# Kernel tuning notes

Measured on AMD Instinct MI355X. Metric: run time of the kernel, lower is better.

## Reference

```python
import jax, jax.numpy as jnp
import numpy as np

N_NODES = 100000
N_EDGES = 1600000
N_GRAPHS = 256
F_IN = 128
HID = 128


def gcn_conv(x, W, b, src, dst, n_nodes):
    """PyG GCNConv: h = D^{-1/2}(A+I)D^{-1/2} (x @ W) + b, self-loops added."""
    h = x @ W  # [N, H]
    ones = jnp.ones((src.shape[0],), dtype=x.dtype)
    deg = jax.ops.segment_sum(ones, dst, num_segments=n_nodes) + 1.0  # +1 self-loop
    dinv = jax.lax.rsqrt(deg)  # deg >= 1 always
    norm = dinv[src] * dinv[dst]  # [E]
    msgs = h[src] * norm[:, None]  # gather + scale, [E, H]
    agg = jax.ops.segment_sum(msgs, dst, num_segments=n_nodes)  # scatter-add
    agg = agg + h * (dinv * dinv)[:, None]  # self-loop contribution
    return agg + b


def setup_inputs() -> dict:
    key = jax.random.key(0)
    ks = jax.random.split(key, 8)
    x = jax.random.normal(ks[0], (N_NODES, F_IN), dtype=jnp.float32)
    edge_index = jax.random.randint(ks[1], (2, N_EDGES), 0, N_NODES, dtype=jnp.int64)
    batch = jnp.sort(jax.random.randint(ks[2], (N_NODES,), 0, N_GRAPHS, dtype=jnp.int64))
    s1 = 1.0 / np.sqrt(F_IN)
    s2 = 1.0 / np.sqrt(HID)
    w1 = jax.random.normal(ks[3], (F_IN, HID), dtype=jnp.float32) * s1
    b1 = jnp.zeros((HID,), dtype=jnp.float32)
    w2 = jax.random.normal(ks[4], (HID, HID), dtype=jnp.float32) * s2
    b2 = jnp.zeros((HID,), dtype=jnp.float32)
    w_out = jax.random.normal(ks[5], (HID, 1), dtype=jnp.float32) * s2
    b_out = jnp.zeros((1,), dtype=jnp.float32)
    return {"x": x, "edge_index": edge_index, "batch": batch,
            "w1": w1, "b1": b1, "w2": w2, "b2": b2,
            "w_out": w_out, "b_out": b_out}


def reference(x, edge_index, batch, w1, b1, w2, b2, w_out, b_out):
    src, dst = edge_index[0], edge_index[1]
    n = x.shape[0]
    h = jax.nn.relu(gcn_conv(x, w1, b1, src, dst, n))
    h = jax.nn.relu(gcn_conv(h, w2, b2, src, dst, n))
    # global mean pool over graphs
    sums = jax.ops.segment_sum(h, batch, num_segments=N_GRAPHS)  # [G, H]
    counts = jax.ops.segment_sum(jnp.ones((n,), dtype=h.dtype), batch, num_segments=N_GRAPHS)
    pooled = sums / jnp.maximum(counts, 1.0)[:, None]
    return pooled @ w_out + b_out  # [G, 1]
```

## Files before the change

### kernel.cpp

```cpp
#include <hip/hip_runtime.h>
#include <hip/hip_fp16.h>

#define N_NODES 100000
#define N_EDGES 1600000
#define N_GRAPHS 256
#define NB 1563
#define SBLOCKS 256
#define GB1 782

typedef _Float16 half8 __attribute__((ext_vector_type(8)));
typedef float f32x4 __attribute__((ext_vector_type(4)));

__device__ __forceinline__ unsigned pack2(float a, float b) {
    __half2 h = __floats2half2_rn(a, b);
    return *reinterpret_cast<unsigned*>(&h);
}

__global__ __launch_bounds__(256) void wprep_kernel(const float* __restrict__ W1,
                                                    const float* __restrict__ W2,
                                                    __half* __restrict__ Wt1,
                                                    __half* __restrict__ Wt2) {
    int b = blockIdx.x;
    const float* W = (b < 64) ? W1 : W2;
    __half* Wt = (b < 64) ? Wt1 : Wt2;
    int t = (b & 63) * 256 + threadIdx.x;
    int n = t >> 7, k = t & 127;
    Wt[t] = (__half)W[k * 128 + n];
}

__global__ __launch_bounds__(256) void gemmhist_kernel(const float* __restrict__ Xf,
                                                       const __half* __restrict__ Xh,
                                                       const __half* __restrict__ Wt,
                                                       const float* __restrict__ dinv,
                                                       __half* __restrict__ HT,
                                                       int xf16, int withDinv,
                                                       const int* __restrict__ dst,
                                                       int* __restrict__ cnt2d,
                                                       int histBlocks) {
    __shared__ __align__(16) char smem[69632];
    const int tid = threadIdx.x;
    int bid = blockIdx.x;
    bool isHist = false;
    int id = bid;
    if (histBlocks) {
        if (bid < 1024) {
            if ((bid & 3) == 0) { isHist = true; id = bid >> 2; }
            else id = (bid >> 2) * 3 + (bid & 3) - 1;
        } else {
            id = 768 + (bid - 1024);
        }
    }

    if (isHist) {
        int* lcnt = (int*)smem;
        for (int i = tid; i < NB; i += 256) lcnt[i] = 0;
        __syncthreads();
        const int per = (N_EDGES + SBLOCKS - 1) / SBLOCKS;
        int e0 = id * per, e1 = min(e0 + per, N_EDGES);
        for (int e = e0 + tid; e < e1; e += 256)
            atomicAdd(&lcnt[dst[e] >> 6], 1);
        __syncthreads();
        for (int i = tid; i < NB; i += 256)
            cnt2d[id * NB + i] = lcnt[i];
        return;
    }

    typedef __half (*TileT)[136];
    TileT Xl = (TileT)smem;
    TileT Wl = (TileT)(smem + 34816);
    const int row0 = id * 128;

#pragma unroll
    for (int i = 0; i < 8; ++i) {
        int idx = tid + i * 256;
        int n = idx >> 4, c0 = (idx & 15) * 8;
        *(uint4*)&Wl[n][c0] = *(const uint4*)&Wt[n * 128 + c0];
    }
    if (xf16) {
#pragma unroll
        for (int i = 0; i < 8; ++i) {
            int idx = tid + i * 256;
            int r = idx >> 4, c0 = (idx & 15) * 8;
            int rr = min(row0 + r, N_NODES - 1);
            *(uint4*)&Xl[r][c0] = *(const uint4*)&Xh[(size_t)rr * 128 + c0];
        }
    } else {
#pragma unroll
        for (int i = 0; i < 16; ++i) {
            int idx = tid + i * 256;
            int r = idx >> 5, c0 = (idx & 31) * 4;
            int rr = min(row0 + r, N_NODES - 1);
            float4 v = *(const float4*)&Xf[(size_t)rr * 128 + c0];
            uint2 o;
            o.x = pack2(v.x, v.y);
            o.y = pack2(v.z, v.w);
            *(uint2*)&Xl[r][c0] = o;
        }
    }
    __syncthreads();

    const int wv = tid >> 6;
    const int lane = tid & 63;
    const int lr = lane & 15;
    const int lg = lane >> 4;

    f32x4 acc[2][8];
#pragma unroll
    for (int mt = 0; mt < 2; ++mt)
#pragma unroll
        for (int nt = 0; nt < 8; ++nt) acc[mt][nt] = (f32x4){0.f, 0.f, 0.f, 0.f};

#pragma unroll
    for (int ks = 0; ks < 4; ++ks) {
        const int kb = ks * 32 + lg * 8;
        half8 a0 = *reinterpret_cast<const half8*>(&Xl[wv * 32 + lr][kb]);
        half8 a1 = *reinterpret_cast<const half8*>(&Xl[wv * 32 + 16 + lr][kb]);
        half8 b[8];
#pragma unroll
        for (int nt = 0; nt < 8; ++nt)
            b[nt] = *reinterpret_cast<const half8*>(&Wl[nt * 16 + lr][kb]);
#pragma unroll
        for (int nt = 0; nt < 8; ++nt) {
            acc[0][nt] = __builtin_amdgcn_mfma_f32_16x16x32_f16(a0, b[nt], acc[0][nt], 0, 0, 0);
            acc[1][nt] = __builtin_amdgcn_mfma_f32_16x16x32_f16(a1, b[nt], acc[1][nt], 0, 0, 0);
        }
    }

#pragma unroll
    for (int mt = 0; mt < 2; ++mt) {
#pragma unroll
        for (int i = 0; i < 4; ++i) {
            int rr = row0 + wv * 32 + mt * 16 + lg * 4 + i;
            if (rr < N_NODES) {
                float di = withDinv ? dinv[rr] : 1.0f;
#pragma unroll
                for (int nt = 0; nt < 8; ++nt)
                    HT[(size_t)rr * 128 + nt * 16 + lr] = (__half)(acc[mt][nt][i] * di);
            }
        }
    }
}

__global__ __launch_bounds__(256) void scan2d_kernel(int* __restrict__ cnt2d,
                                                     int* __restrict__ bucket_cnt) {
    __shared__ int ts[256];
    int i = blockIdx.x;
    int t = threadIdx.x;
    int v = cnt2d[t * NB + i];
    ts[t] = v;
    __syncthreads();
    for (int off = 1; off < 256; off <<= 1) {
        int y = (t >= off) ? ts[t - off] : 0;
        __syncthreads();
        ts[t] += y;
        __syncthreads();
    }
    cnt2d[t * NB + i] = ts[t] - v;
    if (t == 255) bucket_cnt[i] = ts[255];
}

#define BVPT 7
__global__ __launch_bounds__(256) void scanB_kernel(const int* __restrict__ bucket_cnt,
                                                    int* __restrict__ bucket_off) {
    __shared__ int tsum[256];
    int tid = threadIdx.x;
    int v[BVPT];
    int s = 0;
#pragma unroll
    for (int j = 0; j < BVPT; ++j) {
        int idx = tid * BVPT + j;
        v[j] = (idx < NB) ? bucket_cnt[idx] : 0;
        s += v[j];
    }
    tsum[tid] = s;
    __syncthreads();
    for (int off = 1; off < 256; off <<= 1) {
        int y = (tid >= off) ? tsum[tid - off] : 0;
        __syncthreads();
        tsum[tid] += y;
        __syncthreads();
    }
    int run = (tid > 0) ? tsum[tid - 1] : 0;
#pragma unroll
    for (int j = 0; j < BVPT; ++j) {
        int idx = tid * BVPT + j;
        if (idx < NB) bucket_off[idx] = run;
        run += v[j];
    }
    if (tid == 255) bucket_off[NB] = tsum[255];
}

__global__ __launch_bounds__(256) void scatter_kernel(const int* __restrict__ src,
                                                      const int* __restrict__ dst,
                                                      const int* __restrict__ cnt2d,
                                                      const int* __restrict__ bucket_off,
                                                      unsigned* __restrict__ pairbuf) {
    __shared__ int lcur[NB];
    const int tid = threadIdx.x;
    const int blk = blockIdx.x;
    for (int i = tid; i < NB; i += 256)
        lcur[i] = bucket_off[i] + cnt2d[blk * NB + i];
    __syncthreads();
    const int per = (N_EDGES + SBLOCKS - 1) / SBLOCKS;
    int e0 = blk * per, e1 = min(e0 + per, N_EDGES);
    for (int e = e0 + tid; e < e1; e += 256) {
        int d = dst[e];
        int b = d >> 6;
        int p = atomicAdd(&lcur[b], 1);
        pairbuf[p] = ((unsigned)(d & 63) << 17) | (unsigned)src[e];
    }
}

__global__ __launch_bounds__(256) void localsort_kernel(const unsigned* __restrict__ pairbuf,
                                                        const int* __restrict__ bucket_off,
                                                        int* __restrict__ csr_src,
                                                        int* __restrict__ row_off,
                                                        float* __restrict__ dinv) {
    __shared__ int ldeg[64];
    __shared__ int loff[64];
    __shared__ int lcur[64];
    int tid = threadIdx.x;
    int b = blockIdx.x;
    int base = bucket_off[b];
    int cnt = bucket_off[b + 1] - base;
    const unsigned* pb = pairbuf + base;
    int n0 = b << 6;

    if (tid < 64) ldeg[tid] = 0;
    __syncthreads();
    for (int i = tid; i < cnt; i += 256)
        atomicAdd(&ldeg[pb[i] >> 17], 1);
    __syncthreads();
    if (tid < 64) loff[tid] = ldeg[tid];
    __syncthreads();
    for (int off = 1; off < 64; off <<= 1) {
        int y = 0;
        if (tid < 64 && tid >= off) y = loff[tid - off];
        __syncthreads();
        if (tid < 64) loff[tid] += y;
        __syncthreads();
    }
    if (tid < 64) {
        int ex = loff[tid] - ldeg[tid];
        lcur[tid] = ex;
        int n = n0 + tid;
        if (n < N_NODES) {
            row_off[n] = base + ex;
            dinv[n] = rsqrtf((float)ldeg[tid] + 1.0f);
        }
    }
    __syncthreads();
    for (int i = tid; i < cnt; i += 256) {
        unsigned w = pb[i];
        int dl = w >> 17;
        int s = (int)(w & 0x1FFFFu);
        int p = atomicAdd(&lcur[dl], 1);
        csr_src[base + p] = s;
    }
}

__device__ __forceinline__ void add8(float* a, uint4 w) {
    float2 p0 = __half22float2(*reinterpret_cast<__half2*>(&w.x));
    float2 p1 = __half22float2(*reinterpret_cast<__half2*>(&w.y));
    float2 p2 = __half22float2(*reinterpret_cast<__half2*>(&w.z));
    float2 p3 = __half22float2(*reinterpret_cast<__half2*>(&w.w));
    a[0] += p0.x; a[1] += p0.y; a[2] += p1.x; a[3] += p1.y;
    a[4] += p2.x; a[5] += p2.y; a[6] += p3.x; a[7] += p3.y;
}
__device__ __forceinline__ void fma8(float* a, uint4 w, float s) {
    float2 p0 = __half22float2(*reinterpret_cast<__half2*>(&w.x));
    float2 p1 = __half22float2(*reinterpret_cast<__half2*>(&w.y));
    float2 p2 = __half22float2(*reinterpret_cast<__half2*>(&w.z));
    float2 p3 = __half22float2(*reinterpret_cast<__half2*>(&w.w));
    a[0] = fmaf(s, p0.x, a[0]); a[1] = fmaf(s, p0.y, a[1]);
    a[2] = fmaf(s, p1.x, a[2]); a[3] = fmaf(s, p1.y, a[3]);
    a[4] = fmaf(s, p2.x, a[4]); a[5] = fmaf(s, p2.y, a[5]);
    a[6] = fmaf(s, p3.x, a[6]); a[7] = fmaf(s, p3.y, a[7]);
}
template<bool DV>
__global__ __launch_bounds__(256) void gather_kernel(const int* __restrict__ row_off,
                                                     const int* __restrict__ csr_src,
                                                     const __half* __restrict__ ht,
                                                     const float* __restrict__ dinv,
                                                     const float* __restrict__ bias,
                                                     __half* __restrict__ Y) {
    int t = blockIdx.x * 256 + threadIdx.x;
    int n = t >> 4;
    if (n >= N_NODES) return;
    int f = (t & 15) * 8;
    int e0 = row_off[n];
    int e1 = (n < N_NODES - 1) ? row_off[n + 1] : N_EDGES;
    const __half* htf = ht + f;
    float dn = dinv[n];

    float a0[8] = {0,0,0,0,0,0,0,0};
    float a1[8] = {0,0,0,0,0,0,0,0};
    float a2[8] = {0,0,0,0,0,0,0,0};
    float a3[8] = {0,0,0,0,0,0,0,0};
    {
        uint4 w = *(const uint4*)&htf[(size_t)n * 128];
        if (DV) fma8(a0, w, dn); else add8(a0, w);
    }
    int e = e0;
    for (; e + 4 <= e1; e += 4) {
        int s0 = csr_src[e], s1 = csr_src[e + 1];
        int s2 = csr_src[e + 2], s3 = csr_src[e + 3];
        uint4 w0 = *(const uint4*)&htf[(size_t)s0 * 128];
        uint4 w1 = *(const uint4*)&htf[(size_t)s1 * 128];
        uint4 w2 = *(const uint4*)&htf[(size_t)s2 * 128];
        uint4 w3 = *(const uint4*)&htf[(size_t)s3 * 128];
        if (DV) {
            fma8(a0, w0, dinv[s0]); fma8(a1, w1, dinv[s1]);
            fma8(a2, w2, dinv[s2]); fma8(a3, w3, dinv[s3]);
        } else {
            add8(a0, w0); add8(a1, w1); add8(a2, w2); add8(a3, w3);
        }
    }
    for (; e < e1; ++e) {
        int s = csr_src[e];
        uint4 w = *(const uint4*)&htf[(size_t)s * 128];
        if (DV) fma8(a0, w, dinv[s]); else add8(a0, w);
    }

    float4 bb0 = *(const float4*)&bias[f];
    float4 bb1 = *(const float4*)&bias[f + 4];
    float r0 = fmaxf((a0[0]+a1[0]+a2[0]+a3[0]) * dn + bb0.x, 0.0f);
    float r1 = fmaxf((a0[1]+a1[1]+a2[1]+a3[1]) * dn + bb0.y, 0.0f);
    float r2 = fmaxf((a0[2]+a1[2]+a2[2]+a3[2]) * dn + bb0.z, 0.0f);
    float r3 = fmaxf((a0[3]+a1[3]+a2[3]+a3[3]) * dn + bb0.w, 0.0f);
    float r4 = fmaxf((a0[4]+a1[4]+a2[4]+a3[4]) * dn + bb1.x, 0.0f);
    float r5 = fmaxf((a0[5]+a1[5]+a2[5]+a3[5]) * dn + bb1.y, 0.0f);
    float r6 = fmaxf((a0[6]+a1[6]+a2[6]+a3[6]) * dn + bb1.z, 0.0f);
    float r7 = fmaxf((a0[7]+a1[7]+a2[7]+a3[7]) * dn + bb1.w, 0.0f);
    uint4 o;
    o.x = pack2(r0, r1);
    o.y = pack2(r2, r3);
    o.z = pack2(r4, r5);
    o.w = pack2(r6, r7);
    *(uint4*)&Y[(size_t)n * 128 + f] = o;
}

__global__ __launch_bounds__(256) void poolout_kernel(const __half* __restrict__ Y,
                                                      const int* __restrict__ batch,
                                                      const float* __restrict__ w_out,
                                                      const float* __restrict__ b_out,
                                                      float* __restrict__ out) {
    __shared__ float red[8][128];
    __shared__ float pr[128];
    int g = blockIdx.x;
    int tid = threadIdx.x;
    int lo = 0, hi = N_NODES;
    while (lo < hi) { int m = (lo + hi) >> 1; if (batch[m] < g) lo = m + 1; else hi = m; }
    int lo2 = lo, hi2 = N_NODES;
    while (lo2 < hi2) { int m = (lo2 + hi2) >> 1; if (batch[m] < g + 1) lo2 = m + 1; else hi2 = m; }
    int cnt = lo2 - lo;

    int rslot = tid >> 5;
    int f = (tid & 31) * 4;
    float4 acc = make_float4(0, 0, 0, 0);
    for (int n = lo + rslot; n < lo2; n += 8) {
        uint2 w = *(const uint2*)&Y[(size_t)n * 128 + f];
        float2 p0 = __half22float2(*reinterpret_cast<__half2*>(&w.x));
        float2 p1 = __half22float2(*reinterpret_cast<__half2*>(&w.y));
        acc.x += p0.x; acc.y += p0.y; acc.z += p1.x; acc.w += p1.y;
    }
    *(float4*)&red[rslot][f] = acc;
    __syncthreads();
    if (tid < 128) {
        float s = 0.0f;
#pragma unroll
        for (int r = 0; r < 8; ++r) s += red[r][tid];
        pr[tid] = s * w_out[tid];
    }
    __syncthreads();
    for (int off = 64; off >= 1; off >>= 1) {
        if (tid < off) pr[tid] += pr[tid + off];
        __syncthreads();
    }
    if (tid == 0)
        out[g] = pr[0] / fmaxf((float)cnt, 1.0f) + b_out[0];
}

extern "C" void kernel_launch(void* const* d_in, const int* in_sizes, int n_in,
                              void* d_out, int out_size, void* d_ws, size_t ws_size,
                              hipStream_t stream) {
    const float* x     = (const float*)d_in[0];
    const int*   edge  = (const int*)d_in[1];
    const int*   batch = (const int*)d_in[2];
    const float* w1    = (const float*)d_in[3];
    const float* b1    = (const float*)d_in[4];
    const float* w2    = (const float*)d_in[5];
    const float* b2    = (const float*)d_in[6];
    const float* w_out = (const float*)d_in[7];
    const float* b_out = (const float*)d_in[8];
    float* out = (float*)d_out;

    char* ws = (char*)d_ws;
    size_t off = 0;
    auto alloc = [&](size_t bytes) {
        void* p = ws + off;
        off += (bytes + 511) & ~(size_t)511;
        return p;
    };
    const size_t FEAT_BYTES = (size_t)N_NODES * 128 * 4;
    __half*   ht16       = (__half*)alloc(FEAT_BYTES / 2);
    __half*   y16        = (__half*)alloc(FEAT_BYTES / 2);
    unsigned* pairbuf    = (unsigned*)y16;
    float*    dinv       = (float*)alloc(N_NODES * 4);
    int*      row_off    = (int*)alloc(N_NODES * 4);
    int*      csr_src    = (int*)alloc(N_EDGES * 4);
    int*      cnt2d      = (int*)alloc((size_t)SBLOCKS * NB * 4);
    int*      bucket_cnt = (int*)alloc((NB + 1) * 4);
    int*      bucket_off = (int*)alloc((NB + 1) * 4);
    __half*   wt1        = (__half*)alloc(128 * 128 * 2);
    __half*   wt2        = (__half*)alloc(128 * 128 * 2);

    const int* src = edge;
    const int* dst = edge + N_EDGES;

    wprep_kernel<<<128, 256, 0, stream>>>(w1, w2, wt1, wt2);

    gemmhist_kernel<<<1024 + (GB1 - 768), 256, 0, stream>>>(
        x, (const __half*)nullptr, wt1, (const float*)nullptr, ht16,
        0, 0, dst, cnt2d, 1);

    scan2d_kernel<<<NB, 256, 0, stream>>>(cnt2d, bucket_cnt);
    scanB_kernel<<<1, 256, 0, stream>>>(bucket_cnt, bucket_off);
    scatter_kernel<<<SBLOCKS, 256, 0, stream>>>(src, dst, cnt2d, bucket_off, pairbuf);
    localsort_kernel<<<NB, 256, 0, stream>>>(pairbuf, bucket_off, csr_src, row_off, dinv);

    gather_kernel<true><<<(N_NODES * 16 + 255) / 256, 256, 0, stream>>>(
        row_off, csr_src, ht16, dinv, b1, y16);

    gemmhist_kernel<<<GB1, 256, 0, stream>>>(
        (const float*)nullptr, y16, wt2, dinv, ht16, 1, 1,
        (const int*)nullptr, (int*)nullptr, 0);
    gather_kernel<false><<<(N_NODES * 16 + 255) / 256, 256, 0, stream>>>(
        row_off, csr_src, ht16, dinv, b2, y16);

    poolout_kernel<<<N_GRAPHS, 256, 0, stream>>>(y16, batch, w_out, b_out, out);
}
```

Before: 236.0 us.

## Drop LDS tiling in GEMM, halve histogram blocks, rework scan and scatter

```diff
diff --git a/kernel.cpp b/kernel.cpp
--- a/kernel.cpp
+++ b/kernel.cpp
@@ -5,7 +5,7 @@
 #define N_EDGES 1600000
 #define N_GRAPHS 256
 #define NB 1563
-#define SBLOCKS 256
+#define SBLOCKS 128
 #define GB1 782
 
 typedef _Float16 half8 __attribute__((ext_vector_type(8)));
@@ -37,22 +37,20 @@
                                                        const int* __restrict__ dst,
                                                        int* __restrict__ cnt2d,
                                                        int histBlocks) {
-    __shared__ __align__(16) char smem[69632];
+    __shared__ int lcnt[NB];
     const int tid = threadIdx.x;
     int bid = blockIdx.x;
     bool isHist = false;
     int id = bid;
     if (histBlocks) {
-        if (bid < 1024) {
-            if ((bid & 3) == 0) { isHist = true; id = bid >> 2; }
-            else id = (bid >> 2) * 3 + (bid & 3) - 1;
-        } else {
-            id = 768 + (bid - 1024);
+        if ((bid & 7) == 0) { isHist = true; id = bid >> 3; }
+        else {
+            id = (bid >> 3) * 7 + (bid & 7) - 1;
+            if (id >= GB1) return;
         }
     }
 
     if (isHist) {
-        int* lcnt = (int*)smem;
         for (int i = tid; i < NB; i += 256) lcnt[i] = 0;
         __syncthreads();
         const int per = (N_EDGES + SBLOCKS - 1) / SBLOCKS;
@@ -65,44 +63,13 @@
         return;
     }
 
-    typedef __half (*TileT)[136];
-    TileT Xl = (TileT)smem;
-    TileT Wl = (TileT)(smem + 34816);
     const int row0 = id * 128;
-
-#pragma unroll
-    for (int i = 0; i < 8; ++i) {
-        int idx = tid + i * 256;
-        int n = idx >> 4, c0 = (idx & 15) * 8;
-        *(uint4*)&Wl[n][c0] = *(const uint4*)&Wt[n * 128 + c0];
-    }
-    if (xf16) {
-#pragma unroll
-        for (int i = 0; i < 8; ++i) {
-            int idx = tid + i * 256;
-            int r = idx >> 4, c0 = (idx & 15) * 8;
-            int rr = min(row0 + r, N_NODES - 1);
-            *(uint4*)&Xl[r][c0] = *(const uint4*)&Xh[(size_t)rr * 128 + c0];
-        }
-    } else {
-#pragma unroll
-        for (int i = 0; i < 16; ++i) {
-            int idx = tid + i * 256;
-            int r = idx >> 5, c0 = (idx & 31) * 4;
-            int rr = min(row0 + r, N_NODES - 1);
-            float4 v = *(const float4*)&Xf[(size_t)rr * 128 + c0];
-            uint2 o;
-            o.x = pack2(v.x, v.y);
-            o.y = pack2(v.z, v.w);
-            *(uint2*)&Xl[r][c0] = o;
-        }
-    }
-    __syncthreads();
-
     const int wv = tid >> 6;
     const int lane = tid & 63;
     const int lr = lane & 15;
     const int lg = lane >> 4;
+    const int r0 = min(row0 + wv * 32 + lr, N_NODES - 1);
+    const int r1 = min(row0 + wv * 32 + 16 + lr, N_NODES - 1);
 
     f32x4 acc[2][8];
 #pragma unroll
@@ -113,12 +80,28 @@
 #pragma unroll
     for (int ks = 0; ks < 4; ++ks) {
         const int kb = ks * 32 + lg * 8;
-        half8 a0 = *reinterpret_cast<const half8*>(&Xl[wv * 32 + lr][kb]);
-        half8 a1 = *reinterpret_cast<const half8*>(&Xl[wv * 32 + 16 + lr][kb]);
+        half8 a0, a1;
+        if (xf16) {
+            a0 = *reinterpret_cast<const half8*>(&Xh[(size_t)r0 * 128 + kb]);
+            a1 = *reinterpret_cast<const half8*>(&Xh[(size_t)r1 * 128 + kb]);
+        } else {
+            float4 v0 = *(const float4*)&Xf[(size_t)r0 * 128 + kb];
+            float4 v1 = *(const float4*)&Xf[(size_t)r0 * 128 + kb + 4];
+            float4 u0 = *(const float4*)&Xf[(size_t)r1 * 128 + kb];
+            float4 u1 = *(const float4*)&Xf[(size_t)r1 * 128 + kb + 4];
+            a0[0] = (_Float16)v0.x; a0[1] = (_Float16)v0.y;
+            a0[2] = (_Float16)v0.z; a0[3] = (_Float16)v0.w;
+            a0[4] = (_Float16)v1.x; a0[5] = (_Float16)v1.y;
+            a0[6] = (_Float16)v1.z; a0[7] = (_Float16)v1.w;
+            a1[0] = (_Float16)u0.x; a1[1] = (_Float16)u0.y;
+            a1[2] = (_Float16)u0.z; a1[3] = (_Float16)u0.w;
+            a1[4] = (_Float16)u1.x; a1[5] = (_Float16)u1.y;
+            a1[6] = (_Float16)u1.z; a1[7] = (_Float16)u1.w;
+        }
         half8 b[8];
 #pragma unroll
         for (int nt = 0; nt < 8; ++nt)
-            b[nt] = *reinterpret_cast<const half8*>(&Wl[nt * 16 + lr][kb]);
+            b[nt] = *reinterpret_cast<const half8*>(&Wt[(size_t)(nt * 16 + lr) * 128 + kb]);
 #pragma unroll
         for (int nt = 0; nt < 8; ++nt) {
             acc[0][nt] = __builtin_amdgcn_mfma_f32_16x16x32_f16(a0, b[nt], acc[0][nt], 0, 0, 0);
@@ -144,19 +127,22 @@
 __global__ __launch_bounds__(256) void scan2d_kernel(int* __restrict__ cnt2d,
                                                      int* __restrict__ bucket_cnt) {
     __shared__ int ts[256];
-    int i = blockIdx.x;
     int t = threadIdx.x;
-    int v = cnt2d[t * NB + i];
+    int j = t & 127;
+    int bucket = blockIdx.x * 2 + (t >> 7);
+    int v = (bucket < NB) ? cnt2d[j * NB + bucket] : 0;
     ts[t] = v;
     __syncthreads();
-    for (int off = 1; off < 256; off <<= 1) {
-        int y = (t >= off) ? ts[t - off] : 0;
+    for (int off = 1; off < 128; off <<= 1) {
+        int y = (j >= off) ? ts[t - off] : 0;
         __syncthreads();
         ts[t] += y;
         __syncthreads();
     }
-    cnt2d[t * NB + i] = ts[t] - v;
-    if (t == 255) bucket_cnt[i] = ts[255];
+    if (bucket < NB) {
+        cnt2d[j * NB + bucket] = ts[t] - v;
+        if (j == 127) bucket_cnt[bucket] = ts[t];
+    }
 }
 
 #define BVPT 7
@@ -190,20 +176,20 @@
     if (tid == 255) bucket_off[NB] = tsum[255];
 }
 
-__global__ __launch_bounds__(256) void scatter_kernel(const int* __restrict__ src,
-                                                      const int* __restrict__ dst,
-                                                      const int* __restrict__ cnt2d,
-                                                      const int* __restrict__ bucket_off,
-                                                      unsigned* __restrict__ pairbuf) {
+__global__ __launch_bounds__(1024) void scatter_kernel(const int* __restrict__ src,
+                                                       const int* __restrict__ dst,
+                                                       const int* __restrict__ cnt2d,
+                                                       const int* __restrict__ bucket_off,
+                                                       unsigned* __restrict__ pairbuf) {
     __shared__ int lcur[NB];
     const int tid = threadIdx.x;
     const int blk = blockIdx.x;
-    for (int i = tid; i < NB; i += 256)
+    for (int i = tid; i < NB; i += 1024)
         lcur[i] = bucket_off[i] + cnt2d[blk * NB + i];
     __syncthreads();
     const int per = (N_EDGES + SBLOCKS - 1) / SBLOCKS;
     int e0 = blk * per, e1 = min(e0 + per, N_EDGES);
-    for (int e = e0 + tid; e < e1; e += 256) {
+    for (int e = e0 + tid; e < e1; e += 1024) {
         int d = dst[e];
         int b = d >> 6;
         int p = atomicAdd(&lcur[b], 1);
@@ -217,7 +203,6 @@
                                                         int* __restrict__ row_off,
                                                         float* __restrict__ dinv) {
     __shared__ int ldeg[64];
-    __shared__ int loff[64];
     __shared__ int lcur[64];
     int tid = threadIdx.x;
     int b = blockIdx.x;
@@ -231,22 +216,20 @@
     for (int i = tid; i < cnt; i += 256)
         atomicAdd(&ldeg[pb[i] >> 17], 1);
     __syncthreads();
-    if (tid < 64) loff[tid] = ldeg[tid];
-    __syncthreads();
-    for (int off = 1; off < 64; off <<= 1) {
-        int y = 0;
-        if (tid < 64 && tid >= off) y = loff[tid - off];
-        __syncthreads();
-        if (tid < 64) loff[tid] += y;
-        __syncthreads();
-    }
     if (tid < 64) {
-        int ex = loff[tid] - ldeg[tid];
+        int d = ldeg[tid];
+        int x = d;
+#pragma unroll
+        for (int off = 1; off < 64; off <<= 1) {
+            int y = __shfl_up(x, off);
+            if (tid >= off) x += y;
+        }
+        int ex = x - d;
         lcur[tid] = ex;
         int n = n0 + tid;
         if (n < N_NODES) {
             row_off[n] = base + ex;
-            dinv[n] = rsqrtf((float)ldeg[tid] + 1.0f);
+            dinv[n] = rsqrtf((float)d + 1.0f);
         }
     }
     __syncthreads();
@@ -420,13 +403,13 @@
 
     wprep_kernel<<<128, 256, 0, stream>>>(w1, w2, wt1, wt2);
 
-    gemmhist_kernel<<<1024 + (GB1 - 768), 256, 0, stream>>>(
+    gemmhist_kernel<<<1024, 256, 0, stream>>>(
         x, (const __half*)nullptr, wt1, (const float*)nullptr, ht16,
         0, 0, dst, cnt2d, 1);
 
-    scan2d_kernel<<<NB, 256, 0, stream>>>(cnt2d, bucket_cnt);
+    scan2d_kernel<<<(NB + 1) / 2, 256, 0, stream>>>(cnt2d, bucket_cnt);
     scanB_kernel<<<1, 256, 0, stream>>>(bucket_cnt, bucket_off);
-    scatter_kernel<<<SBLOCKS, 256, 0, stream>>>(src, dst, cnt2d, bucket_off, pairbuf);
+    scatter_kernel<<<SBLOCKS, 1024, 0, stream>>>(src, dst, cnt2d, bucket_off, pairbuf);
     localsort_kernel<<<NB, 256, 0, stream>>>(pairbuf, bucket_off, csr_src, row_off, dinv);
 
     gather_kernel<true><<<(N_NODES * 16 + 255) / 256, 256, 0, stream>>>(
```

After: 252.2 us. 1.07x slower.
